# Performance work log

Measured on AMD Instinct MI355X. Metric: run time of the kernel, lower is better.

Reference implementation:

```python
import jax, jax.numpy as jnp
import numpy as np

K = 2048  # num_embeddings
D = 64    # embedding_dim


def setup_inputs() -> dict:
    key = jax.random.key(0)
    k1, k2 = jax.random.split(key)
    inputs = jax.random.normal(k1, (64, 32, 32, D), dtype=jnp.float32)
    # tf.random_uniform_initializer default: U[0, 1)
    embeddings = jax.random.uniform(k2, (K, D), dtype=jnp.float32)
    return {"inputs": inputs, "embeddings": embeddings}


def reference(inputs, embeddings):
    input_shape = inputs.shape
    flat_inputs = inputs.reshape(-1, D)  # [N, D]
    distances = (
        jnp.sum(flat_inputs ** 2, axis=1, keepdims=True)
        - 2.0 * jnp.matmul(flat_inputs, embeddings.T)
        + jnp.sum(embeddings ** 2, axis=1)
    )
    encoding_indices = jnp.argmin(distances, axis=1)  # [N]
    quantized = embeddings[encoding_indices].reshape(input_shape)
    # straight-through estimator
    quantized = inputs + jax.lax.stop_gradient(quantized - inputs)
    return quantized, encoding_indices, flat_inputs
```

## Files before the change

kernel.cpp:

```cpp
#include <hip/hip_runtime.h>
#include <cfloat>

#define N_TOTAL 65536
#define DIM     64
#define NEMB    2048

typedef __attribute__((ext_vector_type(8))) _Float16 half8;
typedef __attribute__((ext_vector_type(4))) float    floatx4;

__global__ void prep_kernel(const float* __restrict__ emb,
                            half8* __restrict__ ehp, float* __restrict__ en) {
    const int t = blockIdx.x * 256 + threadIdx.x;
    {
        const int l   = t & 63;
        const int ks  = (t >> 6) & 1;
        const int g   = t >> 7;
        const int col = g * 16 + (l & 15);
        const int kb  = ks * 32 + (l >> 4) * 8;
        const float* s = emb + col * DIM + kb;
        float4 v0 = *(const float4*)s, v1 = *(const float4*)(s + 4);
        half8 hv;
        hv[0] = (_Float16)v0.x; hv[1] = (_Float16)v0.y;
        hv[2] = (_Float16)v0.z; hv[3] = (_Float16)v0.w;
        hv[4] = (_Float16)v1.x; hv[5] = (_Float16)v1.y;
        hv[6] = (_Float16)v1.z; hv[7] = (_Float16)v1.w;
        ehp[t] = hv;
    }
    if (t < NEMB * 4) {
        const int row = t >> 2, seg = t & 3;
        const float* s = emb + row * DIM + seg * 16;
        float acc = 0.f;
#pragma unroll
        for (int i = 0; i < 4; ++i) {
            float4 v = ((const float4*)s)[i];
            acc = fmaf(v.x, v.x, acc); acc = fmaf(v.y, v.y, acc);
            acc = fmaf(v.z, v.z, acc); acc = fmaf(v.w, v.w, acc);
        }
        acc += __shfl_xor(acc, 1, 64);
        acc += __shfl_xor(acc, 2, 64);
        if (seg == 0) en[row] = acc;
    }
}

__global__ __launch_bounds__(256, 4) void vq_mfma_kernel(
        const float* __restrict__ x, const float* __restrict__ emb,
        const char* __restrict__ ehb, const float* __restrict__ eng,
        float* __restrict__ quant, float* __restrict__ idxf,
        float* __restrict__ flat) {

    __shared__ uint4 Mrg[2][64];

    const int t    = threadIdx.x;
    const int wave = t >> 6, lane = t & 63;
    const int n = lane & 15, q = lane >> 4;
    const int h = wave & 1, p = wave >> 1;
    const int blk0 = blockIdx.x * 64;
    const int row0 = blk0 + p * 32;

    {
        const float4* s4 = (const float4*)(x + (size_t)blk0 * DIM);
        float4*       d4 = (float4*)(flat + (size_t)blk0 * DIM);
#pragma unroll
        for (int i = 0; i < 4; ++i) d4[i * 256 + t] = s4[i * 256 + t];
    }

    half8 ah[2][2], al[2][2];
#pragma unroll
    for (int tl = 0; tl < 2; ++tl)
#pragma unroll
        for (int ks = 0; ks < 2; ++ks) {
            const float* pp = x + (size_t)(row0 + tl * 16 + n) * DIM + ks * 32 + q * 8;
            float4 v0 = *(const float4*)pp, v1 = *(const float4*)(pp + 4);
            float xv[8] = {v0.x, v0.y, v0.z, v0.w, v1.x, v1.y, v1.z, v1.w};
#pragma unroll
            for (int j = 0; j < 8; ++j) {
                _Float16 hh = (_Float16)xv[j];
                ah[tl][ks][j] = hh;
                al[tl][ks][j] = (_Float16)(xv[j] - (float)hh);
            }
        }

    unsigned maskv;
    asm("v_mov_b32 %0, 0xFFFFFFC0" : "=v"(maskv));

    unsigned best[8], sec[8];
#pragma unroll
    for (int r = 0; r < 8; ++r) { best[r] = 0u; sec[r] = 0u; }

    const char*  ebase = ehb + (size_t)h * 131072 + (size_t)lane * 16;
    const float* enp   = eng + h * 1024 + n;

    half8 bbuf[2][4];
    float enc[2][2];
#pragma unroll
    for (int i = 0; i < 4; ++i)
        bbuf[0][i] = *(const half8*)(ebase + i * 1024);
    enc[0][0] = enp[0];
    enc[0][1] = enp[16];

#pragma unroll 2
    for (int tile = 0; tile < 32; ++tile) {
        const int buf = tile & 1;
        if (tile < 31) {
            const char* src = ebase + (size_t)(tile + 1) * 4096;
#pragma unroll
            for (int i = 0; i < 4; ++i)
                bbuf[buf ^ 1][i] = *(const half8*)(src + i * 1024);
            enc[buf ^ 1][0] = enp[(tile + 1) * 32];
            enc[buf ^ 1][1] = enp[(tile + 1) * 32 + 16];
        }

#pragma unroll
        for (int sub = 0; sub < 2; ++sub) {
            const int L = tile * 2 + sub;
            const float enh = fmaf(-0.5f, enc[buf][sub], 128.0f);
            floatx4 e4 = {enh, enh, enh, enh};
            half8 bk0 = bbuf[buf][sub * 2 + 0];
            half8 bk1 = bbuf[buf][sub * 2 + 1];
            __builtin_amdgcn_s_setprio(1);
            floatx4 a0 = __builtin_amdgcn_mfma_f32_16x16x32_f16(ah[0][0], bk0, e4, 0, 0, 0);
            floatx4 a1 = __builtin_amdgcn_mfma_f32_16x16x32_f16(ah[1][0], bk0, e4, 0, 0, 0);
            a0 = __builtin_amdgcn_mfma_f32_16x16x32_f16(al[0][0], bk0, a0, 0, 0, 0);
            a1 = __builtin_amdgcn_mfma_f32_16x16x32_f16(al[1][0], bk0, a1, 0, 0, 0);
            a0 = __builtin_amdgcn_mfma_f32_16x16x32_f16(ah[0][1], bk1, a0, 0, 0, 0);
            a1 = __builtin_amdgcn_mfma_f32_16x16x32_f16(ah[1][1], bk1, a1, 0, 0, 0);
            a0 = __builtin_amdgcn_mfma_f32_16x16x32_f16(al[0][1], bk1, a0, 0, 0, 0);
            a1 = __builtin_amdgcn_mfma_f32_16x16x32_f16(al[1][1], bk1, a1, 0, 0, 0);
            __builtin_amdgcn_s_setprio(0);

            const unsigned Lp = (unsigned)(63 - L);
#pragma unroll
            for (int r = 0; r < 8; ++r) {
                float v = (r < 4) ? a0[r] : a1[r - 4];
                unsigned key = (__float_as_uint(v) & maskv) | Lp;
                unsigned nb  = best[r] > key ? best[r] : key;
                unsigned ns;
                asm("v_med3_u32 %0, %1, %2, %3"
                    : "=v"(ns) : "v"(best[r]), "v"(sec[r]), "v"(key));
                sec[r]  = ns;
                best[r] = nb;
            }
        }
    }

    unsigned bval[8], bcol[8], sval[8], scol[8];
#pragma unroll
    for (int r = 0; r < 8; ++r) {
        bval[r] = best[r] & 0xFFFFFFC0u;
        bcol[r] = (unsigned)(h * 1024 + (63 - (int)(best[r] & 63u)) * 16 + n);
        sval[r] = sec[r] & 0xFFFFFFC0u;
        scol[r] = (unsigned)(h * 1024 + (63 - (int)(sec[r] & 63u)) * 16 + n);
    }
#pragma unroll
    for (int m = 1; m < 16; m <<= 1) {
#pragma unroll
        for (int r = 0; r < 8; ++r) {
            unsigned ov  = (unsigned)__shfl_xor((int)bval[r], m, 64);
            unsigned oc  = (unsigned)__shfl_xor((int)bcol[r], m, 64);
            unsigned ov2 = (unsigned)__shfl_xor((int)sval[r], m, 64);
            unsigned oc2 = (unsigned)__shfl_xor((int)scol[r], m, 64);
            bool ow = (ov > bval[r]) || (ov == bval[r] && oc < bcol[r]);
            unsigned nbv = ow ? ov : bval[r], nbc = ow ? oc : bcol[r];
            unsigned lv  = ow ? bval[r] : ov, lc  = ow ? bcol[r] : oc;
            bool sv2 = (ov2 > sval[r]) || (ov2 == sval[r] && oc2 < scol[r]);
            unsigned bsv = sv2 ? ov2 : sval[r], bsc = sv2 ? oc2 : scol[r];
            bool s3 = (lv > bsv) || (lv == bsv && lc < bsc);
            sval[r] = s3 ? lv : bsv; scol[r] = s3 ? lc : bsc;
            bval[r] = nbv; bcol[r] = nbc;
        }
    }
    if (n == 0) {
#pragma unroll
        for (int r = 0; r < 8; ++r) {
            const int lr = p * 32 + (r >> 2) * 16 + q * 4 + (r & 3);
            Mrg[h][lr] = make_uint4(bval[r], bcol[r], sval[r], scol[r]);
        }
    }
    __syncthreads();

#pragma unroll
    for (int r = 0; r < 4; ++r) {
        const int lr   = wave * 16 + q * 4 + r;
        const int grow = blk0 + lr;
        uint4 c0v = Mrg[0][lr], c1v = Mrg[1][lr];
        int cand[4] = {(int)c0v.y, (int)c0v.w, (int)c1v.y, (int)c1v.w};
        float4 xv = *(const float4*)(x + (size_t)grow * DIM + n * 4);
        float pbest = -FLT_MAX; int cbest = 0;
        float4 ebest = {0.f, 0.f, 0.f, 0.f};
#pragma unroll
        for (int c = 0; c < 4; ++c) {
            float4 e = *(const float4*)(emb + (size_t)cand[c] * DIM + n * 4);
            float pp = (xv.x - 0.5f * e.x) * e.x + (xv.y - 0.5f * e.y) * e.y
                     + (xv.z - 0.5f * e.z) * e.z + (xv.w - 0.5f * e.w) * e.w;
#pragma unroll
            for (int m2 = 1; m2 < 16; m2 <<= 1) pp += __shfl_xor(pp, m2, 64);
            bool take = (pp > pbest) || (pp == pbest && cand[c] < cbest);
            pbest = take ? pp : pbest;
            cbest = take ? cand[c] : cbest;
            ebest.x = take ? e.x : ebest.x; ebest.y = take ? e.y : ebest.y;
            ebest.z = take ? e.z : ebest.z; ebest.w = take ? e.w : ebest.w;
        }
        *(float4*)(quant + (size_t)grow * DIM + n * 4) = ebest;
        if (n == 0) idxf[grow] = (float)cbest;
    }
}

extern "C" void kernel_launch(void* const* d_in, const int* in_sizes, int n_in,
                              void* d_out, int out_size, void* d_ws, size_t ws_size,
                              hipStream_t stream) {
    const float* x   = (const float*)d_in[0];
    const float* emb = (const float*)d_in[1];
    float* out   = (float*)d_out;
    float* quant = out;
    float* idxf  = out + (size_t)N_TOTAL * DIM;
    float* flat  = idxf + N_TOTAL;

    half8* ehp = (half8*)d_ws;
    float* en  = (float*)((char*)d_ws + (size_t)NEMB * DIM * 2);

    prep_kernel<<<64, 256, 0, stream>>>(emb, ehp, en);
    vq_mfma_kernel<<<N_TOTAL / 64, 256, 0, stream>>>(x, emb, (const char*)ehp, en,
                                                     quant, idxf, flat);
}
```

Baseline: 120.0 us.

## Halve rows per block to 32 and stream codebook per 16-column step

Each block now handles 32 rows instead of 64, so every wave computes a single 16-row tile and keeps fewer A fragments and best/second-best registers. This allows launch bounds of 8 blocks per CU and doubles the grid. The codebook loop now runs over 64 single 16-column steps with a two-deep register prefetch, in place of 32 tiles that each covered two steps. The aim is higher occupancy and better latency hiding. The cost is that every codebook fragment is now read from global/L2 twice as often overall, and each MFMA chain has less independent work to interleave.

```diff
diff --git a/kernel.cpp b/kernel.cpp
--- a/kernel.cpp
+++ b/kernel.cpp
@@ -42,110 +42,98 @@
     }
 }
 
-__global__ __launch_bounds__(256, 4) void vq_mfma_kernel(
+__global__ __launch_bounds__(256, 8) void vq_mfma_kernel(
         const float* __restrict__ x, const float* __restrict__ emb,
         const char* __restrict__ ehb, const float* __restrict__ eng,
         float* __restrict__ quant, float* __restrict__ idxf,
         float* __restrict__ flat) {
 
-    __shared__ uint4 Mrg[2][64];
+    __shared__ uint4 Mrg[2][32];
 
     const int t    = threadIdx.x;
     const int wave = t >> 6, lane = t & 63;
     const int n = lane & 15, q = lane >> 4;
     const int h = wave & 1, p = wave >> 1;
-    const int blk0 = blockIdx.x * 64;
-    const int row0 = blk0 + p * 32;
+    const int blk0 = blockIdx.x * 32;
+    const int row0 = blk0 + p * 16;
 
     {
         const float4* s4 = (const float4*)(x + (size_t)blk0 * DIM);
         float4*       d4 = (float4*)(flat + (size_t)blk0 * DIM);
 #pragma unroll
-        for (int i = 0; i < 4; ++i) d4[i * 256 + t] = s4[i * 256 + t];
-    }
-
-    half8 ah[2][2], al[2][2];
-#pragma unroll
-    for (int tl = 0; tl < 2; ++tl)
-#pragma unroll
-        for (int ks = 0; ks < 2; ++ks) {
-            const float* pp = x + (size_t)(row0 + tl * 16 + n) * DIM + ks * 32 + q * 8;
-            float4 v0 = *(const float4*)pp, v1 = *(const float4*)(pp + 4);
-            float xv[8] = {v0.x, v0.y, v0.z, v0.w, v1.x, v1.y, v1.z, v1.w};
-#pragma unroll
-            for (int j = 0; j < 8; ++j) {
-                _Float16 hh = (_Float16)xv[j];
-                ah[tl][ks][j] = hh;
-                al[tl][ks][j] = (_Float16)(xv[j] - (float)hh);
-            }
-        }
+        for (int i = 0; i < 2; ++i) d4[i * 256 + t] = s4[i * 256 + t];
+    }
+
+    half8 ah[2], al[2];
+#pragma unroll
+    for (int ks = 0; ks < 2; ++ks) {
+        const float* pp = x + (size_t)(row0 + n) * DIM + ks * 32 + q * 8;
+        float4 v0 = *(const float4*)pp, v1 = *(const float4*)(pp + 4);
+        float xv[8] = {v0.x, v0.y, v0.z, v0.w, v1.x, v1.y, v1.z, v1.w};
+#pragma unroll
+        for (int j = 0; j < 8; ++j) {
+            _Float16 hh = (_Float16)xv[j];
+            ah[ks][j] = hh;
+            al[ks][j] = (_Float16)(xv[j] - (float)hh);
+        }
+    }
 
     unsigned maskv;
     asm("v_mov_b32 %0, 0xFFFFFFC0" : "=v"(maskv));
 
-    unsigned best[8], sec[8];
-#pragma unroll
-    for (int r = 0; r < 8; ++r) { best[r] = 0u; sec[r] = 0u; }
+    unsigned best[4], sec[4];
+#pragma unroll
+    for (int r = 0; r < 4; ++r) { best[r] = 0u; sec[r] = 0u; }
 
     const char*  ebase = ehb + (size_t)h * 131072 + (size_t)lane * 16;
     const float* enp   = eng + h * 1024 + n;
 
-    half8 bbuf[2][4];
-    float enc[2][2];
-#pragma unroll
-    for (int i = 0; i < 4; ++i)
-        bbuf[0][i] = *(const half8*)(ebase + i * 1024);
-    enc[0][0] = enp[0];
-    enc[0][1] = enp[16];
+    half8 sbuf[2][2];
+    float enc[2];
+#pragma unroll
+    for (int j = 0; j < 2; ++j) {
+        const char* src = ebase + (size_t)j * 2048;
+        sbuf[j][0] = *(const half8*)(src);
+        sbuf[j][1] = *(const half8*)(src + 1024);
+        enc[j]     = enp[j * 16];
+    }
 
 #pragma unroll 2
-    for (int tile = 0; tile < 32; ++tile) {
-        const int buf = tile & 1;
-        if (tile < 31) {
-            const char* src = ebase + (size_t)(tile + 1) * 4096;
-#pragma unroll
-            for (int i = 0; i < 4; ++i)
-                bbuf[buf ^ 1][i] = *(const half8*)(src + i * 1024);
-            enc[buf ^ 1][0] = enp[(tile + 1) * 32];
-            enc[buf ^ 1][1] = enp[(tile + 1) * 32 + 16];
-        }
-
-#pragma unroll
-        for (int sub = 0; sub < 2; ++sub) {
-            const int L = tile * 2 + sub;
-            const float enh = fmaf(-0.5f, enc[buf][sub], 128.0f);
-            floatx4 e4 = {enh, enh, enh, enh};
-            half8 bk0 = bbuf[buf][sub * 2 + 0];
-            half8 bk1 = bbuf[buf][sub * 2 + 1];
-            __builtin_amdgcn_s_setprio(1);
-            floatx4 a0 = __builtin_amdgcn_mfma_f32_16x16x32_f16(ah[0][0], bk0, e4, 0, 0, 0);
-            floatx4 a1 = __builtin_amdgcn_mfma_f32_16x16x32_f16(ah[1][0], bk0, e4, 0, 0, 0);
-            a0 = __builtin_amdgcn_mfma_f32_16x16x32_f16(al[0][0], bk0, a0, 0, 0, 0);
-            a1 = __builtin_amdgcn_mfma_f32_16x16x32_f16(al[1][0], bk0, a1, 0, 0, 0);
-            a0 = __builtin_amdgcn_mfma_f32_16x16x32_f16(ah[0][1], bk1, a0, 0, 0, 0);
-            a1 = __builtin_amdgcn_mfma_f32_16x16x32_f16(ah[1][1], bk1, a1, 0, 0, 0);
-            a0 = __builtin_amdgcn_mfma_f32_16x16x32_f16(al[0][1], bk1, a0, 0, 0, 0);
-            a1 = __builtin_amdgcn_mfma_f32_16x16x32_f16(al[1][1], bk1, a1, 0, 0, 0);
-            __builtin_amdgcn_s_setprio(0);
-
-            const unsigned Lp = (unsigned)(63 - L);
-#pragma unroll
-            for (int r = 0; r < 8; ++r) {
-                float v = (r < 4) ? a0[r] : a1[r - 4];
-                unsigned key = (__float_as_uint(v) & maskv) | Lp;
-                unsigned nb  = best[r] > key ? best[r] : key;
-                unsigned ns;
-                asm("v_med3_u32 %0, %1, %2, %3"
-                    : "=v"(ns) : "v"(best[r]), "v"(sec[r]), "v"(key));
-                sec[r]  = ns;
-                best[r] = nb;
-            }
-        }
-    }
-
-    unsigned bval[8], bcol[8], sval[8], scol[8];
-#pragma unroll
-    for (int r = 0; r < 8; ++r) {
+    for (int i = 0; i < 64; ++i) {
+        const int buf = i & 1;
+
+        const float enh = fmaf(-0.5f, enc[buf], 128.0f);
+        floatx4 e4 = {enh, enh, enh, enh};
+        __builtin_amdgcn_s_setprio(1);
+        floatx4 a0 = __builtin_amdgcn_mfma_f32_16x16x32_f16(ah[0], sbuf[buf][0], e4, 0, 0, 0);
+        a0 = __builtin_amdgcn_mfma_f32_16x16x32_f16(al[0], sbuf[buf][0], a0, 0, 0, 0);
+        a0 = __builtin_amdgcn_mfma_f32_16x16x32_f16(ah[1], sbuf[buf][1], a0, 0, 0, 0);
+        a0 = __builtin_amdgcn_mfma_f32_16x16x32_f16(al[1], sbuf[buf][1], a0, 0, 0, 0);
+        __builtin_amdgcn_s_setprio(0);
+
+        if (i < 62) {
+            const char* src = ebase + (size_t)(i + 2) * 2048;
+            sbuf[buf][0] = *(const half8*)(src);
+            sbuf[buf][1] = *(const half8*)(src + 1024);
+            enc[buf]     = enp[(i + 2) * 16];
+        }
+
+        const unsigned Lp = (unsigned)(63 - i);
+#pragma unroll
+        for (int r = 0; r < 4; ++r) {
+            unsigned key = (__float_as_uint(a0[r]) & maskv) | Lp;
+            unsigned nb  = best[r] > key ? best[r] : key;
+            unsigned ns;
+            asm("v_med3_u32 %0, %1, %2, %3"
+                : "=v"(ns) : "v"(best[r]), "v"(sec[r]), "v"(key));
+            sec[r]  = ns;
+            best[r] = nb;
+        }
+    }
+
+    unsigned bval[4], bcol[4], sval[4], scol[4];
+#pragma unroll
+    for (int r = 0; r < 4; ++r) {
         bval[r] = best[r] & 0xFFFFFFC0u;
         bcol[r] = (unsigned)(h * 1024 + (63 - (int)(best[r] & 63u)) * 16 + n);
         sval[r] = sec[r] & 0xFFFFFFC0u;
@@ -154,7 +142,7 @@
 #pragma unroll
     for (int m = 1; m < 16; m <<= 1) {
 #pragma unroll
-        for (int r = 0; r < 8; ++r) {
+        for (int r = 0; r < 4; ++r) {
             unsigned ov  = (unsigned)__shfl_xor((int)bval[r], m, 64);
             unsigned oc  = (unsigned)__shfl_xor((int)bcol[r], m, 64);
             unsigned ov2 = (unsigned)__shfl_xor((int)sval[r], m, 64);
@@ -171,16 +159,16 @@
     }
     if (n == 0) {
 #pragma unroll
-        for (int r = 0; r < 8; ++r) {
-            const int lr = p * 32 + (r >> 2) * 16 + q * 4 + (r & 3);
+        for (int r = 0; r < 4; ++r) {
+            const int lr = p * 16 + q * 4 + r;
             Mrg[h][lr] = make_uint4(bval[r], bcol[r], sval[r], scol[r]);
         }
     }
     __syncthreads();
 
 #pragma unroll
-    for (int r = 0; r < 4; ++r) {
-        const int lr   = wave * 16 + q * 4 + r;
+    for (int rr = 0; rr < 2; ++rr) {
+        const int lr   = wave * 8 + q * 2 + rr;
         const int grow = blk0 + lr;
         uint4 c0v = Mrg[0][lr], c1v = Mrg[1][lr];
         int cand[4] = {(int)c0v.y, (int)c0v.w, (int)c1v.y, (int)c1v.w};
@@ -219,6 +207,6 @@
     float* en  = (float*)((char*)d_ws + (size_t)NEMB * DIM * 2);
 
     prep_kernel<<<64, 256, 0, stream>>>(emb, ehp, en);
-    vq_mfma_kernel<<<N_TOTAL / 64, 256, 0, stream>>>(x, emb, (const char*)ehp, en,
+    vq_mfma_kernel<<<N_TOTAL / 32, 256, 0, stream>>>(x, emb, (const char*)ehp, en,
                                                      quant, idxf, flat);
 }
```

After: 125.2 us. 1.04x slower.
